# Kernel optimization log

Hardware: AMD Instinct MI355X
Metric: run time of the kernel (lower is better)

Reference implementation:

```python
import jax, jax.numpy as jnp
import numpy as np

B, N, D, H = 2, 512, 64, 128  # batch, tokens, feature dim, hidden (=2*D)
OUT = 64


def setup_inputs() -> dict:
    key = jax.random.key(0)
    ks = jax.random.split(key, 11)
    sH = 1.0 / np.sqrt(H)
    inp = {
        "x": jax.random.normal(ks[0], (B, N, D), dtype=jnp.float32),
        # inner MLP: Linear(2D->H), ReLU, Linear(H->H), ReLU, Linear(H->H)
        "W1": jax.random.normal(ks[1], (2 * D, H), dtype=jnp.float32) / np.sqrt(2 * D),
        "b1": jnp.zeros((H,), jnp.float32),
        "W2": jax.random.normal(ks[2], (H, H), dtype=jnp.float32) * sH,
        "b2": jnp.zeros((H,), jnp.float32),
        "W3": jax.random.normal(ks[3], (H, H), dtype=jnp.float32) * sH,
        "b3": jnp.zeros((H,), jnp.float32),
        # outer MLP: Linear(H->H), ReLU, Linear(H->OUT)
        "V1": jax.random.normal(ks[4], (H, H), dtype=jnp.float32) * sH,
        "c1": jnp.zeros((H,), jnp.float32),
        "V2": jax.random.normal(ks[5], (H, OUT), dtype=jnp.float32) * sH,
        "c2": jnp.zeros((OUT,), jnp.float32),
    }
    return inp


def reference(x, W1, b1, W2, b2, W3, b3, V1, c1, V2, c2):
    d = x.shape[-1]
    # pair[b,i,j] = cat(x[b,j], x[b,i]); fuse cat with first linear:
    # pair @ W1 = x[b,j] @ W1[:d] + x[b,i] @ W1[d:]
    xa = jnp.einsum('bnd,dh->bnh', x, W1[:d])   # contribution of pair_a (index j)
    xb = jnp.einsum('bnd,dh->bnh', x, W1[d:])   # contribution of pair_b (index i)
    h = jax.nn.relu(xa[:, None, :, :] + xb[:, :, None, :] + b1)  # [B,N,N,H]
    h = jax.nn.relu(jnp.einsum('bijh,hk->bijk', h, W2) + b2)
    rel = jnp.einsum('bijh,hk->bijk', h, W3) + b3                # inner output [B,N,N,H]
    pooled = rel.sum(axis=(1, 2))                                # [B,H]
    o = jax.nn.relu(pooled @ V1 + c1)
    return o @ V2 + c2                                           # [B,OUT]
```

## Files before the change

### kernel.cpp

```cpp
#include <hip/hip_runtime.h>
#include <hip/hip_bf16.h>

#define B_ 2
#define N_ 512
#define D_ 64
#define H_ 128
#define OUT_ 64
#define NPAIRS_F 262144.0f

using bf16x8 = __attribute__((ext_vector_type(8))) __bf16;
using f32x4  = __attribute__((ext_vector_type(4))) float;
using f32x2  = __attribute__((ext_vector_type(2))) float;


__device__ __forceinline__ bf16x8 pack_bf16x8(f32x4 u0, f32x4 u1) {
    bf16x8 a;
    #pragma unroll
    for (int t = 0; t < 4; t++) { a[t] = (__bf16)u0[t]; a[t + 4] = (__bf16)u1[t]; }
    return a;
}

__global__ __launch_bounds__(256, 2) void pair_kernel(
    const float* __restrict__ x, const float* __restrict__ W1,
    const float* __restrict__ b1, const float* __restrict__ W2,
    const float* __restrict__ b2, float* __restrict__ P)
{
    const int tid  = threadIdx.x;
    const int lane = tid & 63;
    const int wid  = tid >> 6;
    const int l15  = lane & 15;
    const int quad = lane >> 4;

    const int j0 = blockIdx.x * 16;
    const int i0 = blockIdx.y * 64;
    const int b  = blockIdx.z;

    __shared__ float xbs[64 * H_];
    __shared__ float xas[16 * 132];
    __shared__ float sred[4][H_];

    const f32x4 zero4 = {0.f, 0.f, 0.f, 0.f};

    const float* xiB = x + ((size_t)(b * N_) + i0 + wid * 16 + l15) * D_;
    const float* xjB = x + ((size_t)(b * N_) + j0 + l15) * D_;
    bf16x8 Ai[2], Aj[2];
    #pragma unroll
    for (int s2 = 0; s2 < 2; s2++) {
        const f32x4* pi = (const f32x4*)(xiB + s2 * 32 + quad * 8);
        const f32x4* pj = (const f32x4*)(xjB + s2 * 32 + quad * 8);
        Ai[s2] = pack_bf16x8(pi[0], pi[1]);
        Aj[s2] = pack_bf16x8(pj[0], pj[1]);
    }

    bf16x8 Bb[8][2];
    #pragma unroll
    for (int ct = 0; ct < 8; ct++) {
        #pragma unroll
        for (int s2 = 0; s2 < 2; s2++) {
            f32x4 u0, u1;
            #pragma unroll
            for (int t = 0; t < 4; t++) {
                u0[t] = W1[(64 + s2 * 32 + quad * 8 + t) * H_ + ct * 16 + l15];
                u1[t] = W1[(64 + s2 * 32 + quad * 8 + 4 + t) * H_ + ct * 16 + l15];
            }
            Bb[ct][s2] = pack_bf16x8(u0, u1);
        }
    }
    bf16x8 Ba[2][2];
    #pragma unroll
    for (int e = 0; e < 2; e++) {
        int ct = 2 * wid + e;
        #pragma unroll
        for (int s2 = 0; s2 < 2; s2++) {
            f32x4 u0, u1;
            #pragma unroll
            for (int t = 0; t < 4; t++) {
                u0[t] = W1[(s2 * 32 + quad * 8 + t) * H_ + ct * 16 + l15];
                u1[t] = W1[(s2 * 32 + quad * 8 + 4 + t) * H_ + ct * 16 + l15];
            }
            Ba[e][s2] = pack_bf16x8(u0, u1);
        }
    }

    #pragma unroll
    for (int ct = 0; ct < 8; ct++) {
        f32x4 acc = zero4;
        acc = __builtin_amdgcn_mfma_f32_16x16x32_bf16(Ai[0], Bb[ct][0], acc, 0, 0, 0);
        acc = __builtin_amdgcn_mfma_f32_16x16x32_bf16(Ai[1], Bb[ct][1], acc, 0, 0, 0);
        #pragma unroll
        for (int reg = 0; reg < 4; reg++)
            xbs[(wid * 16 + quad * 4 + reg) * H_ + ct * 16 + l15] = acc[reg];
    }
    #pragma unroll
    for (int e = 0; e < 2; e++) {
        int ct = 2 * wid + e;
        f32x4 acc = zero4;
        acc = __builtin_amdgcn_mfma_f32_16x16x32_bf16(Aj[0], Ba[e][0], acc, 0, 0, 0);
        acc = __builtin_amdgcn_mfma_f32_16x16x32_bf16(Aj[1], Ba[e][1], acc, 0, 0, 0);
        float bv = b1[ct * 16 + l15];
        #pragma unroll
        for (int reg = 0; reg < 4; reg++)
            xas[(quad * 4 + reg) * 132 + ct * 16 + l15] = acc[reg] + bv;
    }

    __builtin_amdgcn_sched_barrier(0);

    bf16x8 bfrag[8][4];
    #pragma unroll
    for (int c = 0; c < 8; c++) {
        #pragma unroll
        for (int s = 0; s < 4; s++) {
            f32x4 u0, u1;
            #pragma unroll
            for (int t = 0; t < 4; t++) {
                u0[t] = W2[(s * 32 + quad * 8 + t) * H_ + c * 16 + l15];
                u1[t] = W2[(s * 32 + quad * 8 + 4 + t) * H_ + c * 16 + l15];
            }
            bfrag[c][s] = pack_bf16x8(u0, u1);
        }
    }

    float nb2[8];
    #pragma unroll
    for (int c = 0; c < 8; c++) nb2[c] = -b2[16 * c + l15];

    __syncthreads();

    f32x4 av[4][2];
    #pragma unroll
    for (int s = 0; s < 4; s++) {
        const f32x4* p = (const f32x4*)(xas + l15 * 132 + s * 32 + quad * 8);
        av[s][0] = p[0];
        av[s][1] = p[1];
    }

    f32x2 csum[8];
    #pragma unroll
    for (int c = 0; c < 8; c++) { csum[c][0] = 0.f; csum[c][1] = 0.f; }

    const float* xrow = xbs + (wid * 16) * H_;

    #pragma unroll 2
    for (int r = 0; r < 16; r++) {
        const float* xr = xrow + r * H_;

        bf16x8 afr[4];
        #pragma unroll
        for (int s = 0; s < 4; s++) {
            const f32x4* p = (const f32x4*)(xr + s * 32 + quad * 8);
            f32x4 f0 = av[s][0] + p[0];
            f32x4 f1 = av[s][1] + p[1];
            f0 = __builtin_elementwise_max(f0, zero4);
            f1 = __builtin_elementwise_max(f1, zero4);
            afr[s] = pack_bf16x8(f0, f1);
        }

        #pragma unroll
        for (int c = 0; c < 8; c++) {
            f32x4 acc = zero4;
            #pragma unroll
            for (int s = 0; s < 4; s++)
                acc = __builtin_amdgcn_mfma_f32_16x16x32_bf16(afr[s], bfrag[c][s], acc, 0, 0, 0);
            f32x2 lo; lo[0] = acc[0]; lo[1] = acc[1];
            f32x2 hi; hi[0] = acc[2]; hi[1] = acc[3];
            f32x2 nb; nb[0] = nb2[c]; nb[1] = nb2[c];
            lo = __builtin_elementwise_max(lo, nb);
            hi = __builtin_elementwise_max(hi, nb);
            csum[c] += lo + hi;
        }
    }

    float redv[8];
    #pragma unroll
    for (int c = 0; c < 8; c++) {
        float v = csum[c][0] + csum[c][1];
        v += __shfl_xor(v, 16, 64);
        v += __shfl_xor(v, 32, 64);
        redv[c] = v;
    }

    if (lane < 16) {
        #pragma unroll
        for (int c = 0; c < 8; c++) sred[wid][c * 16 + l15] = redv[c];
    }
    __syncthreads();
    if (tid < H_) {
        float tot = sred[0][tid] + sred[1][tid] + sred[2][tid] + sred[3][tid];
        int id = blockIdx.x * 8 + blockIdx.y;
        P[((size_t)(b * H_ + tid)) * 256 + id] = tot;
    }
}

__global__ __launch_bounds__(128) void tail_kernel(
    const float* __restrict__ P, const float* __restrict__ b2,
    const float* __restrict__ W3, const float* __restrict__ b3,
    const float* __restrict__ V1, const float* __restrict__ c1,
    const float* __restrict__ V2, const float* __restrict__ c2,
    float* __restrict__ out)
{
    __shared__ float Ss[H_], pool[H_], ov[H_];
    const int b = blockIdx.x, t = threadIdx.x;
    const f32x4* Pr = (const f32x4*)(P + ((size_t)(b * H_ + t)) * 256);
    f32x4 s4 = {0.f, 0.f, 0.f, 0.f};
    #pragma unroll 8
    for (int k = 0; k < 64; k++) s4 += Pr[k];
    Ss[t] = (s4[0] + s4[1] + s4[2] + s4[3]) + NPAIRS_F * b2[t];
    __syncthreads();
    float acc = 0.f;
    for (int k = 0; k < H_; k++) acc += Ss[k] * W3[k * H_ + t];
    pool[t] = acc + NPAIRS_F * b3[t];
    __syncthreads();
    acc = c1[t];
    for (int k = 0; k < H_; k++) acc += pool[k] * V1[k * H_ + t];
    ov[t] = acc > 0.f ? acc : 0.f;
    __syncthreads();
    if (t < OUT_) {
        acc = c2[t];
        for (int k = 0; k < H_; k++) acc += ov[k] * V2[k * OUT_ + t];
        out[b * OUT_ + t] = acc;
    }
}

extern "C" void kernel_launch(void* const* d_in, const int* in_sizes, int n_in,
                              void* d_out, int out_size, void* d_ws, size_t ws_size,
                              hipStream_t stream) {
    const float* x  = (const float*)d_in[0];
    const float* W1 = (const float*)d_in[1];
    const float* b1 = (const float*)d_in[2];
    const float* W2 = (const float*)d_in[3];
    const float* b2 = (const float*)d_in[4];
    const float* W3 = (const float*)d_in[5];
    const float* b3 = (const float*)d_in[6];
    const float* V1 = (const float*)d_in[7];
    const float* c1 = (const float*)d_in[8];
    const float* V2 = (const float*)d_in[9];
    const float* c2 = (const float*)d_in[10];
    float* out = (float*)d_out;

    float* P = (float*)d_ws;

    dim3 g2(N_ / 16, N_ / 64, B_);
    pair_kernel<<<g2, 256, 0, stream>>>(x, W1, b1, W2, b2, P);
    tail_kernel<<<B_, 128, 0, stream>>>(P, b2, W3, b3, V1, c1, V2, c2, out);
}
```

Before: 113.3 us.

## Split pair-kernel waves across output columns and halve i-tile for occupancy

Each block now covers 32 i-rows instead of 64. Its four waves form a 2x2 grid: two groups of 16 rows times two halves of the 128 output columns. That halves the per-wave W2 fragment registers, raises launch_bounds to 4 blocks per CU and doubles the grid, so the tail kernel reduces 512 partials per channel instead of 256. It also reorders the MFMA loop to interleave the four column accumulators, and reads xa values from LDS each iteration instead of keeping them in registers. The cost is that every W2 fragment is loaded by twice as many blocks, there is more LDS traffic per MFMA, and the tail reduction is longer.

```diff
diff --git a/kernel.cpp b/kernel.cpp
--- a/kernel.cpp
+++ b/kernel.cpp
@@ -7,6 +7,7 @@
 #define H_ 128
 #define OUT_ 64
 #define NPAIRS_F 262144.0f
+#define NBLK_ 512
 
 using bf16x8 = __attribute__((ext_vector_type(8))) __bf16;
 using f32x4  = __attribute__((ext_vector_type(4))) float;
@@ -20,28 +21,30 @@
     return a;
 }
 
-__global__ __launch_bounds__(256, 2) void pair_kernel(
+__global__ __launch_bounds__(256, 4) void pair_kernel(
     const float* __restrict__ x, const float* __restrict__ W1,
     const float* __restrict__ b1, const float* __restrict__ W2,
     const float* __restrict__ b2, float* __restrict__ P)
 {
     const int tid  = threadIdx.x;
     const int lane = tid & 63;
-    const int wid  = tid >> 6;
+    const int w    = tid >> 6;
+    const int wi   = w & 1;
+    const int wc   = w >> 1;
     const int l15  = lane & 15;
     const int quad = lane >> 4;
 
     const int j0 = blockIdx.x * 16;
-    const int i0 = blockIdx.y * 64;
+    const int i0 = blockIdx.y * 32;
     const int b  = blockIdx.z;
 
-    __shared__ float xbs[64 * H_];
+    __shared__ float xbs[32 * H_];
     __shared__ float xas[16 * 132];
-    __shared__ float sred[4][H_];
+    __shared__ float sred[2][H_];
 
     const f32x4 zero4 = {0.f, 0.f, 0.f, 0.f};
 
-    const float* xiB = x + ((size_t)(b * N_) + i0 + wid * 16 + l15) * D_;
+    const float* xiB = x + ((size_t)(b * N_) + i0 + wi * 16 + l15) * D_;
     const float* xjB = x + ((size_t)(b * N_) + j0 + l15) * D_;
     bf16x8 Ai[2], Aj[2];
     #pragma unroll
@@ -52,9 +55,10 @@
         Aj[s2] = pack_bf16x8(pj[0], pj[1]);
     }
 
-    bf16x8 Bb[8][2];
-    #pragma unroll
-    for (int ct = 0; ct < 8; ct++) {
+    bf16x8 Bb[4][2];
+    #pragma unroll
+    for (int cc = 0; cc < 4; cc++) {
+        int ct = wc * 4 + cc;
         #pragma unroll
         for (int s2 = 0; s2 < 2; s2++) {
             f32x4 u0, u1;
@@ -63,13 +67,13 @@
                 u0[t] = W1[(64 + s2 * 32 + quad * 8 + t) * H_ + ct * 16 + l15];
                 u1[t] = W1[(64 + s2 * 32 + quad * 8 + 4 + t) * H_ + ct * 16 + l15];
             }
-            Bb[ct][s2] = pack_bf16x8(u0, u1);
+            Bb[cc][s2] = pack_bf16x8(u0, u1);
         }
     }
     bf16x8 Ba[2][2];
     #pragma unroll
     for (int e = 0; e < 2; e++) {
-        int ct = 2 * wid + e;
+        int ct = 2 * w + e;
         #pragma unroll
         for (int s2 = 0; s2 < 2; s2++) {
             f32x4 u0, u1;
@@ -83,17 +87,18 @@
     }
 
     #pragma unroll
-    for (int ct = 0; ct < 8; ct++) {
+    for (int cc = 0; cc < 4; cc++) {
+        int ct = wc * 4 + cc;
         f32x4 acc = zero4;
-        acc = __builtin_amdgcn_mfma_f32_16x16x32_bf16(Ai[0], Bb[ct][0], acc, 0, 0, 0);
-        acc = __builtin_amdgcn_mfma_f32_16x16x32_bf16(Ai[1], Bb[ct][1], acc, 0, 0, 0);
+        acc = __builtin_amdgcn_mfma_f32_16x16x32_bf16(Ai[0], Bb[cc][0], acc, 0, 0, 0);
+        acc = __builtin_amdgcn_mfma_f32_16x16x32_bf16(Ai[1], Bb[cc][1], acc, 0, 0, 0);
         #pragma unroll
         for (int reg = 0; reg < 4; reg++)
-            xbs[(wid * 16 + quad * 4 + reg) * H_ + ct * 16 + l15] = acc[reg];
+            xbs[(wi * 16 + quad * 4 + reg) * H_ + ct * 16 + l15] = acc[reg];
     }
     #pragma unroll
     for (int e = 0; e < 2; e++) {
-        int ct = 2 * wid + e;
+        int ct = 2 * w + e;
         f32x4 acc = zero4;
         acc = __builtin_amdgcn_mfma_f32_16x16x32_bf16(Aj[0], Ba[e][0], acc, 0, 0, 0);
         acc = __builtin_amdgcn_mfma_f32_16x16x32_bf16(Aj[1], Ba[e][1], acc, 0, 0, 0);
@@ -105,9 +110,10 @@
 
     __builtin_amdgcn_sched_barrier(0);
 
-    bf16x8 bfrag[8][4];
-    #pragma unroll
-    for (int c = 0; c < 8; c++) {
+    bf16x8 bfrag[4][4];
+    #pragma unroll
+    for (int cc = 0; cc < 4; cc++) {
+        int c = wc * 4 + cc;
         #pragma unroll
         for (int s = 0; s < 4; s++) {
             f32x4 u0, u1;
@@ -116,78 +122,75 @@
                 u0[t] = W2[(s * 32 + quad * 8 + t) * H_ + c * 16 + l15];
                 u1[t] = W2[(s * 32 + quad * 8 + 4 + t) * H_ + c * 16 + l15];
             }
-            bfrag[c][s] = pack_bf16x8(u0, u1);
-        }
-    }
-
-    float nb2[8];
-    #pragma unroll
-    for (int c = 0; c < 8; c++) nb2[c] = -b2[16 * c + l15];
-
-    __syncthreads();
-
-    f32x4 av[4][2];
-    #pragma unroll
-    for (int s = 0; s < 4; s++) {
-        const f32x4* p = (const f32x4*)(xas + l15 * 132 + s * 32 + quad * 8);
-        av[s][0] = p[0];
-        av[s][1] = p[1];
-    }
-
-    f32x2 csum[8];
-    #pragma unroll
-    for (int c = 0; c < 8; c++) { csum[c][0] = 0.f; csum[c][1] = 0.f; }
-
-    const float* xrow = xbs + (wid * 16) * H_;
+            bfrag[cc][s] = pack_bf16x8(u0, u1);
+        }
+    }
+
+    float nb2[4];
+    #pragma unroll
+    for (int cc = 0; cc < 4; cc++) nb2[cc] = -b2[16 * (wc * 4 + cc) + l15];
+
+    __syncthreads();
+
+    f32x2 csum[4];
+    #pragma unroll
+    for (int cc = 0; cc < 4; cc++) { csum[cc][0] = 0.f; csum[cc][1] = 0.f; }
+
+    const float* xrow  = xbs + (wi * 16) * H_;
+    const float* xarow = xas + l15 * 132;
 
     #pragma unroll 2
     for (int r = 0; r < 16; r++) {
         const float* xr = xrow + r * H_;
 
-        bf16x8 afr[4];
+        f32x4 acc[4];
+        #pragma unroll
+        for (int cc = 0; cc < 4; cc++) acc[cc] = zero4;
+
         #pragma unroll
         for (int s = 0; s < 4; s++) {
-            const f32x4* p = (const f32x4*)(xr + s * 32 + quad * 8);
-            f32x4 f0 = av[s][0] + p[0];
-            f32x4 f1 = av[s][1] + p[1];
+            const f32x4* pA = (const f32x4*)(xarow + s * 32 + quad * 8);
+            const f32x4* pB = (const f32x4*)(xr + s * 32 + quad * 8);
+            f32x4 f0 = pA[0] + pB[0];
+            f32x4 f1 = pA[1] + pB[1];
             f0 = __builtin_elementwise_max(f0, zero4);
             f1 = __builtin_elementwise_max(f1, zero4);
-            afr[s] = pack_bf16x8(f0, f1);
-        }
-
-        #pragma unroll
-        for (int c = 0; c < 8; c++) {
-            f32x4 acc = zero4;
-            #pragma unroll
-            for (int s = 0; s < 4; s++)
-                acc = __builtin_amdgcn_mfma_f32_16x16x32_bf16(afr[s], bfrag[c][s], acc, 0, 0, 0);
-            f32x2 lo; lo[0] = acc[0]; lo[1] = acc[1];
-            f32x2 hi; hi[0] = acc[2]; hi[1] = acc[3];
-            f32x2 nb; nb[0] = nb2[c]; nb[1] = nb2[c];
+            bf16x8 afr = pack_bf16x8(f0, f1);
+            #pragma unroll
+            for (int cc = 0; cc < 4; cc++)
+                acc[cc] = __builtin_amdgcn_mfma_f32_16x16x32_bf16(afr, bfrag[cc][s], acc[cc], 0, 0, 0);
+        }
+
+        #pragma unroll
+        for (int cc = 0; cc < 4; cc++) {
+            f32x2 lo; lo[0] = acc[cc][0]; lo[1] = acc[cc][1];
+            f32x2 hi; hi[0] = acc[cc][2]; hi[1] = acc[cc][3];
+            f32x2 nb; nb[0] = nb2[cc]; nb[1] = nb2[cc];
             lo = __builtin_elementwise_max(lo, nb);
             hi = __builtin_elementwise_max(hi, nb);
-            csum[c] += lo + hi;
-        }
-    }
-
-    float redv[8];
-    #pragma unroll
-    for (int c = 0; c < 8; c++) {
-        float v = csum[c][0] + csum[c][1];
+            csum[cc] += lo + hi;
+        }
+    }
+
+    float redv[4];
+    #pragma unroll
+    for (int cc = 0; cc < 4; cc++) {
+        float v = csum[cc][0] + csum[cc][1];
         v += __shfl_xor(v, 16, 64);
         v += __shfl_xor(v, 32, 64);
-        redv[c] = v;
+        redv[cc] = v;
     }
 
     if (lane < 16) {
         #pragma unroll
-        for (int c = 0; c < 8; c++) sred[wid][c * 16 + l15] = redv[c];
+        for (int cc = 0; cc < 4; cc++)
+            sred[wi][16 * (wc * 4 + cc) + l15] = redv[cc];
     }
     __syncthreads();
     if (tid < H_) {
-        float tot = sred[0][tid] + sred[1][tid] + sred[2][tid] + sred[3][tid];
-        int id = blockIdx.x * 8 + blockIdx.y;
-        P[((size_t)(b * H_ + tid)) * 256 + id] = tot;
+        float tot = sred[0][tid] + sred[1][tid];
+        int id = blockIdx.x * 16 + blockIdx.y;
+        P[((size_t)(b * H_ + tid)) * NBLK_ + id] = tot;
     }
 }
 
@@ -200,10 +203,10 @@
 {
     __shared__ float Ss[H_], pool[H_], ov[H_];
     const int b = blockIdx.x, t = threadIdx.x;
-    const f32x4* Pr = (const f32x4*)(P + ((size_t)(b * H_ + t)) * 256);
+    const f32x4* Pr = (const f32x4*)(P + ((size_t)(b * H_ + t)) * NBLK_);
     f32x4 s4 = {0.f, 0.f, 0.f, 0.f};
     #pragma unroll 8
-    for (int k = 0; k < 64; k++) s4 += Pr[k];
+    for (int k = 0; k < NBLK_ / 4; k++) s4 += Pr[k];
     Ss[t] = (s4[0] + s4[1] + s4[2] + s4[3]) + NPAIRS_F * b2[t];
     __syncthreads();
     float acc = 0.f;
@@ -239,7 +242,7 @@
 
     float* P = (float*)d_ws;
 
-    dim3 g2(N_ / 16, N_ / 64, B_);
+    dim3 g2(N_ / 16, N_ / 32, B_);
     pair_kernel<<<g2, 256, 0, stream>>>(x, W1, b1, W2, b2, P);
     tail_kernel<<<B_, 128, 0, stream>>>(P, b2, W3, b3, V1, c1, V2, c2, out);
 }
```

After: 196.3 us. 1.73x slower.
